# Kernel optimization log

Measured on AMD Instinct MI355X. Metric: run time of the kernel, lower is better.

Reference implementation:

```python
import jax, jax.numpy as jnp
import numpy as np

N_NODES = 50000
N_REL = 8
IN_DIM = 128
HID = 128
N_EDGES = 800000
N_TRIP = 100000


def setup_inputs() -> dict:
    key = jax.random.key(0)
    ks = jax.random.split(key, 12)
    s = 0.05
    return {
        "emb": jax.random.normal(ks[0], (N_NODES, IN_DIM), jnp.float32),
        "W0": jax.random.normal(ks[1], (N_REL, IN_DIM, HID), jnp.float32) * s,
        "root0": jax.random.normal(ks[2], (IN_DIM, HID), jnp.float32) * s,
        "b0": jnp.zeros((HID,), jnp.float32),
        "W1": jax.random.normal(ks[3], (N_REL, HID, HID), jnp.float32) * s,
        "root1": jax.random.normal(ks[4], (HID, HID), jnp.float32) * s,
        "b1": jnp.zeros((HID,), jnp.float32),
        "rel_emb": jax.random.normal(ks[5], (N_REL, HID), jnp.float32),
        "edge_index": jax.random.randint(ks[6], (2, N_EDGES), 0, N_NODES, jnp.int64 if jax.config.read('jax_enable_x64') else jnp.int32),
        "edge_type": jax.random.randint(ks[7], (N_EDGES,), 0, N_REL, jnp.int32),
        "head_idx": jax.random.randint(ks[8], (N_TRIP,), 0, N_NODES, jnp.int32),
        "rel_idx": jax.random.randint(ks[9], (N_TRIP,), 0, N_REL, jnp.int32),
        "tail_idx": jax.random.randint(ks[10], (N_TRIP,), 0, N_NODES, jnp.int32),
    }


def _rgcn_layer(h, W, root, bias, src, dst, edge_type):
    # PyG RGCNConv: per-relation MEAN aggregation of neighbor features at dst,
    # transformed by the relation weight, plus root transform and bias.
    # Mean commutes with the linear map, so aggregate raw features first.
    n, r = N_NODES, N_REL
    seg = dst * r + edge_type  # (E,) joint (dst, relation) segment id
    msg = h[src]               # (E, d) irregular gather
    sums = jax.ops.segment_sum(msg, seg, num_segments=n * r)          # (N*R, d)
    cnt = jax.ops.segment_sum(jnp.ones((src.shape[0],), h.dtype), seg,
                              num_segments=n * r)                     # (N*R,)
    mean = (sums / jnp.maximum(cnt, 1.0)[:, None]).reshape(n, r, -1)  # (N, R, d)
    return jnp.einsum('nrd,rdh->nh', mean, W) + h @ root + bias


def reference(emb, W0, root0, b0, W1, root1, b1, rel_emb,
              edge_index, edge_type, head_idx, rel_idx, tail_idx):
    src = edge_index[0]
    dst = edge_index[1]
    et = edge_type.astype(jnp.int32)
    h = emb
    h = jax.nn.relu(_rgcn_layer(h, W0, root0, b0, src, dst, et))
    h = jax.nn.relu(_rgcn_layer(h, W1, root1, b1, src, dst, et))
    # DistMult score: sum(h_head * r * h_tail)
    score = jnp.sum(h[head_idx] * rel_emb[rel_idx] * h[tail_idx], axis=-1)
    return score
```

## Files before the change

### kernel.cpp

```cpp
#include <hip/hip_runtime.h>
#include <hip/hip_bf16.h>

#define N_NODES 50000
#define N_REL   8
#define DIM     128
#define N_EDGES 800000
#define N_TRIP  100000
#define NSEG    (N_NODES * N_REL)
#define NBUCKET 196
#define CAP     6144

typedef __attribute__((ext_vector_type(8))) short bf16x8;
typedef __attribute__((ext_vector_type(4))) float f32x4;

static __device__ __forceinline__ unsigned short f2b(float f) {
    __hip_bfloat16 h = __float2bfloat16(f);
    return *reinterpret_cast<unsigned short*>(&h);
}
static __device__ __forceinline__ float blo(unsigned int u) {
    return __uint_as_float(u << 16);
}
static __device__ __forceinline__ float bhi(unsigned int u) {
    return __uint_as_float(u & 0xffff0000u);
}
static __device__ __forceinline__ int lds_off(int row, int chunk) {
    return (row * 16 + (chunk ^ (row & 7))) * 8;
}

__global__ __launch_bounds__(256) void bucket_scatter(
        const int* __restrict__ edge_index,
        const int* __restrict__ edge_type,
        int* __restrict__ gcnt,
        unsigned int* __restrict__ slack) {
    __shared__ int hist[NBUCKET];
    __shared__ int cur[NBUCKET];
    int tid = threadIdx.x;
    for (int i = tid; i < NBUCKET; i += 256) hist[i] = 0;
    __syncthreads();
    int base = blockIdx.x * 4096;
    unsigned int w[16];
    int bk[16];
    #pragma unroll
    for (int i = 0; i < 16; ++i) {
        int e = base + i * 256 + tid;
        if (e < N_EDGES) {
            int src = edge_index[e];
            int dst = edge_index[N_EDGES + e];
            int r = edge_type[e];
            w[i] = (unsigned int)src | ((unsigned int)r << 16) |
                   ((unsigned int)(dst & 255) << 19);
            bk[i] = dst >> 8;
            atomicAdd(&hist[bk[i]], 1);
        } else {
            bk[i] = -1;
        }
    }
    __syncthreads();
    for (int i = tid; i < NBUCKET; i += 256)
        cur[i] = atomicAdd(&gcnt[i], hist[i]);
    __syncthreads();
    #pragma unroll
    for (int i = 0; i < 16; ++i) {
        if (bk[i] >= 0) {
            int p = atomicAdd(&cur[bk[i]], 1);
            if (p < CAP) slack[(size_t)bk[i] * CAP + p] = w[i];
        }
    }
}

__global__ void bucket_scan(const int* __restrict__ gcnt,
                            int* __restrict__ gbase,
                            int* __restrict__ offsets) {
    __shared__ int sh[256];
    int t = threadIdx.x;
    int v = (t < NBUCKET) ? gcnt[t] : 0;
    sh[t] = v;
    __syncthreads();
    #pragma unroll
    for (int off = 1; off < 256; off <<= 1) {
        int x = (t >= off) ? sh[t - off] : 0;
        __syncthreads();
        sh[t] += x;
        __syncthreads();
    }
    if (t < NBUCKET) gbase[t] = sh[t] - v;
    if (t == 0) offsets[NSEG] = N_EDGES;
}

__global__ __launch_bounds__(256) void bucket_sort(
        const unsigned int* __restrict__ slack,
        const int* __restrict__ gcnt,
        const int* __restrict__ gbase,
        unsigned int* __restrict__ sorted_pack,
        int* __restrict__ offsets) {
    __shared__ unsigned int ebuf[CAP];
    __shared__ unsigned int obuf[CAP];
    __shared__ int hist[2048];
    __shared__ int excl[2048];
    __shared__ int sh[256];
    int b = blockIdx.x, t = threadIdx.x;
    int n = gcnt[b]; if (n > CAP) n = CAP;
    int bb = gbase[b];
    for (int i = t; i < n; i += 256) ebuf[i] = slack[(size_t)b * CAP + i];
    for (int i = t; i < 2048; i += 256) hist[i] = 0;
    __syncthreads();
    for (int i = t; i < n; i += 256) {
        unsigned int w = ebuf[i];
        int seg = (int)((w >> 19) << 3) | (int)((w >> 16) & 7u);
        atomicAdd(&hist[seg], 1);
    }
    __syncthreads();
    int c[8];
    int s = 0;
    #pragma unroll
    for (int j = 0; j < 8; ++j) { c[j] = hist[t * 8 + j]; s += c[j]; }
    sh[t] = s;
    __syncthreads();
    #pragma unroll
    for (int off = 1; off < 256; off <<= 1) {
        int x = (t >= off) ? sh[t - off] : 0;
        __syncthreads();
        sh[t] += x;
        __syncthreads();
    }
    int ex = sh[t] - s;
    #pragma unroll
    for (int j = 0; j < 8; ++j) { excl[t * 8 + j] = ex; ex += c[j]; }
    __syncthreads();
    #pragma unroll
    for (int j = 0; j < 8; ++j) hist[t * 8 + j] = excl[t * 8 + j];
    __syncthreads();
    for (int i = t; i < n; i += 256) {
        unsigned int w = ebuf[i];
        int seg = (int)((w >> 19) << 3) | (int)((w >> 16) & 7u);
        int p = atomicAdd(&hist[seg], 1);
        obuf[p] = w & 0x7ffffu;
    }
    __syncthreads();
    for (int i = t; i < n; i += 256) sorted_pack[bb + i] = obuf[i];
    int segbase = b * 2048;
    for (int j = t; j < 2048; j += 256) {
        int gseg = segbase + j;
        if (gseg < NSEG) offsets[gseg] = bb + excl[j];
    }
}

__global__ void invcnt_kernel(const int* __restrict__ offsets,
                              float* __restrict__ invcnt) {
    int i = blockIdx.x * blockDim.x + threadIdx.x;
    if (i >= NSEG) return;
    int c = offsets[i + 1] - offsets[i];
    invcnt[i] = (c > 0) ? 1.0f / (float)c : 0.f;
}

__global__ void cvt_emb_kernel(const float* __restrict__ src,
                               unsigned short* __restrict__ dst) {
    int i = blockIdx.x * blockDim.x + threadIdx.x;
    const int npair = N_NODES * DIM / 2;
    if (i >= npair) return;
    float2 v = ((const float2*)src)[i];
    unsigned int p = (unsigned int)f2b(v.x) | ((unsigned int)f2b(v.y) << 16);
    ((unsigned int*)dst)[i] = p;
}

__global__ void cvt_w2_kernel(const float* __restrict__ root,
                              const float* __restrict__ W,
                              unsigned short* __restrict__ Wt2) {
    int s = blockIdx.x;
    int n = blockIdx.y;
    int k = threadIdx.x;
    float v = (s == 0) ? root[k * 128 + n]
                       : W[((size_t)(s - 1) * 128 + k) * 128 + n];
    Wt2[((size_t)s * 128 + n) * 128 + k] = f2b(v);
}

__global__ __launch_bounds__(256) void gemm9_all(
        const unsigned short* __restrict__ hb,
        const unsigned short* __restrict__ Wt2,
        unsigned short* __restrict__ Y) {
    __shared__ unsigned short Bs[128 * 16 * 8];

    int tid = threadIdx.x;
    int wave = tid >> 6, lane = tid & 63;
    int wm = wave & 1, wn = wave >> 1;
    int quad = lane >> 4, l16 = lane & 15;
    int row0 = blockIdx.x * 64;

    bf16x8 afr[2][4];
    #pragma unroll
    for (int i = 0; i < 2; ++i) {
        int grow = row0 + wm * 32 + i * 16 + l16;
        if (grow >= N_NODES) grow = N_NODES - 1;
        #pragma unroll
        for (int kk = 0; kk < 4; ++kk)
            afr[i][kk] = *(const bf16x8*)(hb + (size_t)grow * DIM + kk * 32 + quad * 8);
    }

    for (int s = 0; s < 9; ++s) {
        __syncthreads();
        {
            int n = tid >> 1, c0 = (tid & 1) * 8;
            const unsigned short* gp = Wt2 + ((size_t)s * 128 + n) * 128 + c0 * 8;
            #pragma unroll
            for (int q = 0; q < 8; ++q)
                *(bf16x8*)&Bs[lds_off(n, c0 + q)] = *(const bf16x8*)(gp + q * 8);
        }
        __syncthreads();

        f32x4 acc[2][4];
        #pragma unroll
        for (int i = 0; i < 2; ++i)
            #pragma unroll
            for (int j = 0; j < 4; ++j) acc[i][j] = (f32x4){0.f, 0.f, 0.f, 0.f};

        #pragma unroll
        for (int kk = 0; kk < 4; ++kk) {
            int chunk = kk * 4 + quad;
            bf16x8 bfr[4];
            #pragma unroll
            for (int j = 0; j < 4; ++j)
                bfr[j] = *(const bf16x8*)&Bs[lds_off(wn * 64 + j * 16 + l16, chunk)];
            #pragma unroll
            for (int i = 0; i < 2; ++i)
                #pragma unroll
                for (int j = 0; j < 4; ++j)
                    acc[i][j] = __builtin_amdgcn_mfma_f32_16x16x32_bf16(
                        afr[i][kk], bfr[j], acc[i][j], 0, 0, 0);
        }

        #pragma unroll
        for (int i = 0; i < 2; ++i) {
            int gr0 = row0 + wm * 32 + i * 16 + quad * 4;
            #pragma unroll
            for (int j = 0; j < 4; ++j) {
                int gc = wn * 64 + j * 16 + l16;
                #pragma unroll
                for (int r = 0; r < 4; ++r) {
                    int grow = gr0 + r;
                    if (grow < N_NODES)
                        Y[((size_t)s * N_NODES + grow) * 128 + gc] = f2b(acc[i][j][r]);
                }
            }
        }
    }
}

__global__ __launch_bounds__(256) void aggregate_out(
        const unsigned short* __restrict__ Y,
        const float* __restrict__ bias,
        const int* __restrict__ offsets,
        const unsigned int* __restrict__ sorted_pack,
        const float* __restrict__ invcnt,
        unsigned short* __restrict__ hout) {
    int dst = blockIdx.x * 4 + (threadIdx.x >> 6);
    if (dst >= N_NODES) return;
    int lane = threadIdx.x & 63;
    const unsigned int* Yu = (const unsigned int*)Y;

    unsigned int r0 = Yu[(size_t)dst * 64 + lane];
    float a0 = blo(r0), a1 = bhi(r0);

    int beg = offsets[dst * N_REL];
    int end = offsets[dst * N_REL + N_REL];
    for (int base = beg; base < end; base += 64) {
        int np = end - base; if (np > 64) np = 64;
        unsigned int pk = 0; float ivl = 0.f;
        if (lane < np) {
            pk = sorted_pack[base + lane];
            ivl = invcnt[dst * N_REL + (int)(pk >> 16)];
        }
        int j = 0;
        for (; j + 3 < np; j += 4) {
            unsigned int p0 = __shfl((int)pk, j, 64);
            unsigned int p1 = __shfl((int)pk, j + 1, 64);
            unsigned int p2 = __shfl((int)pk, j + 2, 64);
            unsigned int p3 = __shfl((int)pk, j + 3, 64);
            float i0 = __shfl(ivl, j, 64);
            float i1 = __shfl(ivl, j + 1, 64);
            float i2 = __shfl(ivl, j + 2, 64);
            float i3 = __shfl(ivl, j + 3, 64);
            unsigned int v0 = Yu[((size_t)(1 + (p0 >> 16)) * N_NODES + (p0 & 0xffffu)) * 64 + lane];
            unsigned int v1 = Yu[((size_t)(1 + (p1 >> 16)) * N_NODES + (p1 & 0xffffu)) * 64 + lane];
            unsigned int v2 = Yu[((size_t)(1 + (p2 >> 16)) * N_NODES + (p2 & 0xffffu)) * 64 + lane];
            unsigned int v3 = Yu[((size_t)(1 + (p3 >> 16)) * N_NODES + (p3 & 0xffffu)) * 64 + lane];
            a0 = fmaf(blo(v0), i0, a0); a1 = fmaf(bhi(v0), i0, a1);
            a0 = fmaf(blo(v1), i1, a0); a1 = fmaf(bhi(v1), i1, a1);
            a0 = fmaf(blo(v2), i2, a0); a1 = fmaf(bhi(v2), i2, a1);
            a0 = fmaf(blo(v3), i3, a0); a1 = fmaf(bhi(v3), i3, a1);
        }
        for (; j < np; ++j) {
            unsigned int pj = __shfl((int)pk, j, 64);
            float ij = __shfl(ivl, j, 64);
            unsigned int v = Yu[((size_t)(1 + (pj >> 16)) * N_NODES + (pj & 0xffffu)) * 64 + lane];
            a0 = fmaf(blo(v), ij, a0); a1 = fmaf(bhi(v), ij, a1);
        }
    }
    float2 bv = ((const float2*)bias)[lane];
    a0 = fmaxf(a0 + bv.x, 0.f);
    a1 = fmaxf(a1 + bv.y, 0.f);
    unsigned int po = (unsigned int)f2b(a0) | ((unsigned int)f2b(a1) << 16);
    ((unsigned int*)(hout + (size_t)dst * DIM))[lane] = po;
}

__global__ void score_kernel(const unsigned short* __restrict__ hb,
                             const float* __restrict__ rel_emb,
                             const int* __restrict__ head,
                             const int* __restrict__ rel,
                             const int* __restrict__ tail,
                             float* __restrict__ out) {
    int t = blockIdx.x * 4 + (threadIdx.x >> 6);
    if (t >= N_TRIP) return;
    int lane = threadIdx.x & 63;
    unsigned int ph = ((const unsigned int*)(hb + (size_t)head[t] * DIM))[lane];
    unsigned int pt = ((const unsigned int*)(hb + (size_t)tail[t] * DIM))[lane];
    float2 rr = ((const float2*)(rel_emb + (size_t)rel[t] * DIM))[lane];
    float s = blo(ph) * rr.x * blo(pt) + bhi(ph) * rr.y * bhi(pt);
    #pragma unroll
    for (int off = 32; off; off >>= 1) s += __shfl_xor(s, off, 64);
    if (lane == 0) out[t] = s;
}

extern "C" void kernel_launch(void* const* d_in, const int* in_sizes, int n_in,
                              void* d_out, int out_size, void* d_ws, size_t ws_size,
                              hipStream_t stream) {
    const float* emb     = (const float*)d_in[0];
    const float* W0      = (const float*)d_in[1];
    const float* root0   = (const float*)d_in[2];
    const float* b0      = (const float*)d_in[3];
    const float* W1      = (const float*)d_in[4];
    const float* root1   = (const float*)d_in[5];
    const float* b1      = (const float*)d_in[6];
    const float* rel_emb = (const float*)d_in[7];
    const int* edge_index = (const int*)d_in[8];
    const int* edge_type  = (const int*)d_in[9];
    const int* head_idx   = (const int*)d_in[10];
    const int* rel_idx    = (const int*)d_in[11];
    const int* tail_idx   = (const int*)d_in[12];
    float* out = (float*)d_out;

    char* p = (char*)d_ws;
    size_t y_bytes   = (size_t)9 * N_NODES * DIM * sizeof(unsigned short);
    size_t hb_bytes  = (size_t)N_NODES * DIM * sizeof(unsigned short);
    size_t wt2_bytes = (size_t)9 * 128 * 128 * sizeof(unsigned short);
    unsigned short* Y    = (unsigned short*)p; p += y_bytes;
    unsigned short* embb = (unsigned short*)p; p += hb_bytes;
    unsigned short* h1b  = (unsigned short*)p; p += hb_bytes;
    unsigned short* h2b  = (unsigned short*)p; p += hb_bytes;
    unsigned short* Wt2a = (unsigned short*)p; p += wt2_bytes;
    unsigned short* Wt2b = (unsigned short*)p; p += wt2_bytes;
    int* offsets = (int*)p;           p += (size_t)(NSEG + 1) * sizeof(int);
    float* invcnt = (float*)p;        p += (size_t)NSEG * sizeof(float);
    unsigned int* sorted_pack = (unsigned int*)p; p += (size_t)N_EDGES * sizeof(unsigned int);
    unsigned int* slack = (unsigned int*)p; p += (size_t)NBUCKET * CAP * sizeof(unsigned int);
    int* gcnt  = (int*)p;             p += (size_t)NBUCKET * sizeof(int);
    int* gbase = (int*)p;
    (void)ws_size; (void)in_sizes; (void)n_in; (void)out_size;

    dim3 blk256(256);

    hipMemsetAsync(gcnt, 0, (size_t)NBUCKET * sizeof(int), stream);
    bucket_scatter<<<(N_EDGES + 4095) / 4096, blk256, 0, stream>>>(edge_index, edge_type,
                                                                   gcnt, slack);
    bucket_scan<<<1, 256, 0, stream>>>(gcnt, gbase, offsets);
    bucket_sort<<<NBUCKET, blk256, 0, stream>>>(slack, gcnt, gbase, sorted_pack, offsets);
    invcnt_kernel<<<(NSEG + 255) / 256, blk256, 0, stream>>>(offsets, invcnt);

    cvt_emb_kernel<<<(N_NODES * DIM / 2 + 255) / 256, blk256, 0, stream>>>(emb, embb);
    cvt_w2_kernel<<<dim3(9, 128), 128, 0, stream>>>(root0, W0, Wt2a);
    cvt_w2_kernel<<<dim3(9, 128), 128, 0, stream>>>(root1, W1, Wt2b);

    int ggrid = (N_NODES + 63) / 64;
    int agrid = (N_NODES + 3) / 4;

    gemm9_all<<<ggrid, blk256, 0, stream>>>(embb, Wt2a, Y);
    aggregate_out<<<agrid, blk256, 0, stream>>>(Y, b0, offsets, sorted_pack, invcnt, h1b);

    gemm9_all<<<ggrid, blk256, 0, stream>>>(h1b, Wt2b, Y);
    aggregate_out<<<agrid, blk256, 0, stream>>>(Y, b1, offsets, sorted_pack, invcnt, h2b);

    score_kernel<<<(N_TRIP + 3) / 4, blk256, 0, stream>>>(h2b, rel_emb, head_idx, rel_idx,
                                                          tail_idx, out);
}
```

Before: 339.6 us.

## Stage GEMM output through LDS for coalesced stores; fuse invcnt and weight-convert launches

The GEMM epilogue now writes bf16 results into a padded shared-memory tile and then stores 16-byte vectors per row, replacing the scattered 2-byte global stores. The inverse-count computation is folded into bucket_sort, which reuses its per-thread segment counts, and the two weight-conversion launches are merged into one 3D grid. The goal is lower global store traffic in the GEMM and fewer kernel launches. In exchange the GEMM needs an extra LDS buffer and a barrier per relation slice, which may reduce occupancy.

```diff
diff --git a/kernel.cpp b/kernel.cpp
--- a/kernel.cpp
+++ b/kernel.cpp
@@ -9,6 +9,7 @@
 #define NSEG    (N_NODES * N_REL)
 #define NBUCKET 196
 #define CAP     6144
+#define CPAD    132
 
 typedef __attribute__((ext_vector_type(8))) short bf16x8;
 typedef __attribute__((ext_vector_type(4))) float f32x4;
@@ -92,7 +93,8 @@
         const int* __restrict__ gcnt,
         const int* __restrict__ gbase,
         unsigned int* __restrict__ sorted_pack,
-        int* __restrict__ offsets) {
+        int* __restrict__ offsets,
+        float* __restrict__ invcnt) {
     __shared__ unsigned int ebuf[CAP];
     __shared__ unsigned int obuf[CAP];
     __shared__ int hist[2048];
@@ -139,18 +141,14 @@
     __syncthreads();
     for (int i = t; i < n; i += 256) sorted_pack[bb + i] = obuf[i];
     int segbase = b * 2048;
-    for (int j = t; j < 2048; j += 256) {
-        int gseg = segbase + j;
-        if (gseg < NSEG) offsets[gseg] = bb + excl[j];
-    }
-}
-
-__global__ void invcnt_kernel(const int* __restrict__ offsets,
-                              float* __restrict__ invcnt) {
-    int i = blockIdx.x * blockDim.x + threadIdx.x;
-    if (i >= NSEG) return;
-    int c = offsets[i + 1] - offsets[i];
-    invcnt[i] = (c > 0) ? 1.0f / (float)c : 0.f;
+    #pragma unroll
+    for (int j = 0; j < 8; ++j) {
+        int gseg = segbase + t * 8 + j;
+        if (gseg < NSEG) {
+            offsets[gseg] = bb + excl[t * 8 + j];
+            invcnt[gseg] = (c[j] > 0) ? 1.0f / (float)c[j] : 0.f;
+        }
+    }
 }
 
 __global__ void cvt_emb_kernel(const float* __restrict__ src,
@@ -163,12 +161,18 @@
     ((unsigned int*)dst)[i] = p;
 }
 
-__global__ void cvt_w2_kernel(const float* __restrict__ root,
-                              const float* __restrict__ W,
-                              unsigned short* __restrict__ Wt2) {
+__global__ void cvt_w2_kernel(const float* __restrict__ root0,
+                              const float* __restrict__ W0,
+                              const float* __restrict__ root1,
+                              const float* __restrict__ W1,
+                              unsigned short* __restrict__ Wt2a,
+                              unsigned short* __restrict__ Wt2b) {
     int s = blockIdx.x;
     int n = blockIdx.y;
     int k = threadIdx.x;
+    const float* root = blockIdx.z ? root1 : root0;
+    const float* W    = blockIdx.z ? W1 : W0;
+    unsigned short* Wt2 = blockIdx.z ? Wt2b : Wt2a;
     float v = (s == 0) ? root[k * 128 + n]
                        : W[((size_t)(s - 1) * 128 + k) * 128 + n];
     Wt2[((size_t)s * 128 + n) * 128 + k] = f2b(v);
@@ -179,6 +183,7 @@
         const unsigned short* __restrict__ Wt2,
         unsigned short* __restrict__ Y) {
     __shared__ unsigned short Bs[128 * 16 * 8];
+    __shared__ unsigned short Cs[64 * CPAD];
 
     int tid = threadIdx.x;
     int wave = tid >> 6, lane = tid & 63;
@@ -196,6 +201,10 @@
             afr[i][kk] = *(const bf16x8*)(hb + (size_t)grow * DIM + kk * 32 + quad * 8);
     }
 
+    int er = tid >> 2, ec = (tid & 3) * 32;
+    int egrow = row0 + er;
+    bool estore = (egrow < N_NODES);
+
     for (int s = 0; s < 9; ++s) {
         __syncthreads();
         {
@@ -230,17 +239,21 @@
 
         #pragma unroll
         for (int i = 0; i < 2; ++i) {
-            int gr0 = row0 + wm * 32 + i * 16 + quad * 4;
+            int rb = wm * 32 + i * 16 + quad * 4;
             #pragma unroll
             for (int j = 0; j < 4; ++j) {
-                int gc = wn * 64 + j * 16 + l16;
+                int col = wn * 64 + j * 16 + l16;
                 #pragma unroll
-                for (int r = 0; r < 4; ++r) {
-                    int grow = gr0 + r;
-                    if (grow < N_NODES)
-                        Y[((size_t)s * N_NODES + grow) * 128 + gc] = f2b(acc[i][j][r]);
-                }
+                for (int r = 0; r < 4; ++r)
+                    Cs[(rb + r) * CPAD + col] = f2b(acc[i][j][r]);
             }
+        }
+        __syncthreads();
+        if (estore) {
+            const uint4* cp = (const uint4*)&Cs[er * CPAD + ec];
+            uint4* yp = (uint4*)(Y + ((size_t)s * N_NODES + egrow) * 128 + ec);
+            uint4 v0 = cp[0], v1 = cp[1], v2 = cp[2], v3 = cp[3];
+            yp[0] = v0; yp[1] = v1; yp[2] = v2; yp[3] = v3;
         }
     }
 }
@@ -362,12 +375,11 @@
     bucket_scatter<<<(N_EDGES + 4095) / 4096, blk256, 0, stream>>>(edge_index, edge_type,
                                                                    gcnt, slack);
     bucket_scan<<<1, 256, 0, stream>>>(gcnt, gbase, offsets);
-    bucket_sort<<<NBUCKET, blk256, 0, stream>>>(slack, gcnt, gbase, sorted_pack, offsets);
-    invcnt_kernel<<<(NSEG + 255) / 256, blk256, 0, stream>>>(offsets, invcnt);
+    bucket_sort<<<NBUCKET, blk256, 0, stream>>>(slack, gcnt, gbase, sorted_pack,
+                                                offsets, invcnt);
 
     cvt_emb_kernel<<<(N_NODES * DIM / 2 + 255) / 256, blk256, 0, stream>>>(emb, embb);
-    cvt_w2_kernel<<<dim3(9, 128), 128, 0, stream>>>(root0, W0, Wt2a);
-    cvt_w2_kernel<<<dim3(9, 128), 128, 0, stream>>>(root1, W1, Wt2b);
+    cvt_w2_kernel<<<dim3(9, 128, 2), 128, 0, stream>>>(root0, W0, root1, W1, Wt2a, Wt2b);
 
     int ggrid = (N_NODES + 63) / 64;
     int agrid = (N_NODES + 3) / 4;
```

After: 365.9 us. +7.7%, slower.
